# Kernel tuning notes

Measured on AMD Instinct MI355X. Metric: run time of the kernel, lower is better.

## Reference

```python
import jax, jax.numpy as jnp
import numpy as np

G, S = 4, 2
EPS_GN, EPS_COS = 1e-5, 1e-8


def group_norm(x, w, b, groups):
    B, C, H, W = x.shape
    xg = x.reshape(B, groups, C // groups, H, W)
    m = xg.mean(axis=(2, 3, 4), keepdims=True)
    v = ((xg - m) ** 2).mean(axis=(2, 3, 4), keepdims=True)
    xn = ((xg - m) / jnp.sqrt(v + EPS_GN)).reshape(B, C, H, W)
    return xn * w[None, :, None, None] + b[None, :, None, None]


def compute_similarity(x, k=3, dilation=2):
    # cosine similarity (over channels) between each pixel and its 8 dilated
    # neighbors (zero padded, unfold row-major order, center dropped)
    B, C, H, W = x.shape
    pad = (k // 2) * dilation
    xp = jnp.pad(x, ((0, 0), (0, 0), (pad, pad), (pad, pad)))
    cn = jnp.sqrt(jnp.sum(x * x, axis=1))  # (B,H,W)
    sims = []
    for ki in range(k):
        for kj in range(k):
            if ki == k // 2 and kj == k // 2:
                continue
            nb = jax.lax.dynamic_slice(xp, (0, 0, ki * dilation, kj * dilation), (B, C, H, W))
            dot = jnp.sum(x * nb, axis=1)
            nn_ = jnp.sqrt(jnp.sum(nb * nb, axis=1))
            sims.append(dot / jnp.maximum(cn * nn_, EPS_COS))
    return jnp.stack(sims, axis=1)  # (B, k*k-1, H, W)


def conv1x1_bn(x, w, sc, bi):
    # 1x1 conv (no bias) followed by eval-mode BN folded to per-channel scale/shift
    return jnp.einsum('oc,bchw->bohw', w, x) * sc[None, :, None, None] + bi[None, :, None, None]


def pixel_unshuffle(x, r):
    B, C, H, W = x.shape
    return x.reshape(B, C, H // r, r, W // r, r).transpose(0, 1, 3, 5, 2, 4).reshape(B, C * r * r, H // r, W // r)


def pixel_shuffle(x, r):
    B, C, H, W = x.shape
    return x.reshape(B, C // (r * r), r, r, H, W).transpose(0, 1, 4, 2, 5, 3).reshape(B, C // (r * r), H * r, W * r)


def init_pos(dtype):
    h = jnp.arange((-S + 1) / 2, (S - 1) / 2 + 1, dtype=dtype) / S  # [-0.25, 0.25]
    t = jnp.stack(jnp.meshgrid(h, h, indexing='ij')).transpose(0, 2, 1)  # (2,2,2)
    return jnp.tile(t, (1, G, 1)).reshape(1, -1, 1, 1)  # (1, 2*g*s*s, 1, 1)


def grid_sample_border(x, grid):
    # bilinear, align_corners=False, padding_mode='border'
    N, C, H, W = x.shape
    gx = jnp.clip(((grid[..., 0] + 1) * W - 1) / 2, 0.0, W - 1.0)
    gy = jnp.clip(((grid[..., 1] + 1) * H - 1) / 2, 0.0, H - 1.0)
    x0 = jnp.floor(gx)
    y0 = jnp.floor(gy)
    wx = (gx - x0)[..., None]
    wy = (gy - y0)[..., None]
    x0i = x0.astype(jnp.int32)
    y0i = y0.astype(jnp.int32)
    x1i = jnp.minimum(x0i + 1, W - 1)
    y1i = jnp.minimum(y0i + 1, H - 1)
    bi = jnp.arange(N)[:, None, None]
    v00 = x[bi, :, y0i, x0i]  # (N,Ho,Wo,C)
    v01 = x[bi, :, y0i, x1i]
    v10 = x[bi, :, y1i, x0i]
    v11 = x[bi, :, y1i, x1i]
    out = (v00 * (1 - wx) + v01 * wx) * (1 - wy) + (v10 * (1 - wx) + v11 * wx) * wy
    return out.transpose(0, 3, 1, 2)  # (N,C,Ho,Wo)


def sample(x, offset):
    b, _, h, w = offset.shape
    off = offset.reshape(b, 2, -1, h, w)  # (b,2,g*s*s,h,w)
    cw = jnp.arange(w, dtype=x.dtype) + 0.5
    ch = jnp.arange(h, dtype=x.dtype) + 0.5
    coords = jnp.stack(jnp.meshgrid(cw, ch, indexing='ij')).transpose(0, 2, 1)[None, :, None]  # (1,2,1,h,w)
    norm = jnp.array([w, h], dtype=x.dtype).reshape(1, 2, 1, 1, 1)
    coords = 2 * (coords + off) / norm - 1
    grid = pixel_shuffle(coords.reshape(b, -1, h, w), S)  # (b, 2*g, s*h, s*w)
    grid = grid.reshape(b, 2, G, S * h, S * w).transpose(0, 2, 3, 4, 1).reshape(b * G, S * h, S * w, 2)
    C = x.shape[1]
    out = grid_sample_border(x.reshape(b * G, C // G, h, w), grid)
    return out.reshape(b, C, S * h, S * w)


def setup_inputs() -> dict:
    key = jax.random.key(0)
    ks = jax.random.split(key, 24)
    B, C, H, W, CF = 2, 64, 128, 128, 256
    CIN, C2L, C2H = C + 8, 2 * G * S * S, 2 * G
    f = jnp.float32
    return {
        'x_l': jax.random.normal(ks[0], (B, C, H, W), f),
        'x_h': jax.random.normal(ks[1], (B, C, 2 * H, 2 * W), f),
        'feat2sample': jax.random.normal(ks[2], (B, CF, H, W), f),
        'gn_l_w': 1.0 + 0.1 * jax.random.normal(ks[3], (C,), f),
        'gn_l_b': 0.1 * jax.random.normal(ks[4], (C,), f),
        'gn_h_w': 1.0 + 0.1 * jax.random.normal(ks[5], (C,), f),
        'gn_h_b': 0.1 * jax.random.normal(ks[6], (C,), f),
        'w_off': 0.02 * jax.random.normal(ks[7], (C2L, CIN), f),
        's_off': 1.0 + 0.05 * jax.random.normal(ks[8], (C2L,), f),
        'b_off': 0.02 * jax.random.normal(ks[9], (C2L,), f),
        'w_off_h': 0.02 * jax.random.normal(ks[10], (C2H, CIN), f),
        's_off_h': 1.0 + 0.05 * jax.random.normal(ks[11], (C2H,), f),
        'b_off_h': 0.02 * jax.random.normal(ks[12], (C2H,), f),
        'w_ds': 0.02 * jax.random.normal(ks[13], (C2L, CIN), f),
        's_ds': 1.0 + 0.05 * jax.random.normal(ks[14], (C2L,), f),
        'b_ds': 0.02 * jax.random.normal(ks[15], (C2L,), f),
        'w_ds_h': 0.02 * jax.random.normal(ks[16], (C2H, CIN), f),
        's_ds_h': 1.0 + 0.05 * jax.random.normal(ks[17], (C2H,), f),
        'b_ds_h': 0.02 * jax.random.normal(ks[18], (C2H,), f),
    }


def reference(x_l, x_h, feat2sample, gn_l_w, gn_l_b, gn_h_w, gn_h_b,
              w_off, s_off, b_off, w_off_h, s_off_h, b_off_h,
              w_ds, s_ds, b_ds, w_ds_h, s_ds_h, b_ds_h):
    xl = group_norm(x_l, gn_l_w, gn_l_b, x_l.shape[1] // 8)
    xh = group_norm(x_h, gn_h_w, gn_h_b, x_h.shape[1] // 8)
    sim_l = jnp.concatenate([xl, compute_similarity(xl)], axis=1)  # (B, C+8, H, W)
    sim_h = jnp.concatenate([xh, compute_similarity(xh)], axis=1)  # (B, C+8, 2H, 2W)
    off = conv1x1_bn(sim_l, w_off, s_off, b_off) \
        + pixel_unshuffle(conv1x1_bn(sim_h, w_off_h, s_off_h, b_off_h), S)
    gate = jax.nn.sigmoid(conv1x1_bn(sim_l, w_ds, s_ds, b_ds)
                          + pixel_unshuffle(conv1x1_bn(sim_h, w_ds_h, s_ds_h, b_ds_h), S))
    offset = off * gate + init_pos(xl.dtype)  # (B, 2*g*s*s, H, W)
    return sample(feat2sample, offset)
```

## Files before the change

### kernel.cpp

```cpp
#include <hip/hip_runtime.h>
#include <math.h>

#define BATCH 2
#define CCH 64
#define HL 128
#define WL 128
#define HH 256
#define WH 256
#define CFCH 256
#define CIN 72

constexpr long WS_AL   = 0;
constexpr long WS_BL   = 128;
constexpr long WS_AH   = 256;
constexpr long WS_BH   = 384;
constexpr long WS_OFFL = 512;
constexpr long WS_DSL  = WS_OFFL + 1048576;
constexpr long WS_OFFH = WS_DSL + 1048576;
constexpr long WS_DSH  = WS_OFFH + 1048576;
constexpr long WS_CRD  = WS_DSH + 1048576;
constexpr long WS_PART = WS_CRD + 1048576;

__global__ void k_stats1(const float* __restrict__ xl, const float* __restrict__ xh,
                         float* __restrict__ ws) {
  int blk = blockIdx.x;
  const float* x;
  long base;
  int gg, slice;
  if (blk < 256) {
    int g = blk >> 4; slice = blk & 15;
    x = xl; gg = g;
    base = (long)g * 8 * (HL * WL) + (long)slice * 8192;
  } else {
    int id = blk - 256;
    int g = id >> 6; slice = id & 63;
    x = xh; gg = 16 + g;
    base = (long)g * 8 * (HH * WH) + (long)slice * 8192;
  }
  const float4* p = (const float4*)(x + base);
  float s = 0.f, s2 = 0.f;
  #pragma unroll
  for (int k = 0; k < 8; k++) {
    float4 v = p[threadIdx.x + k * 256];
    s  += v.x + v.y + v.z + v.w;
    s2 += v.x * v.x + v.y * v.y + v.z * v.z + v.w * v.w;
  }
  __shared__ float sh1[256], sh2[256];
  sh1[threadIdx.x] = s; sh2[threadIdx.x] = s2;
  __syncthreads();
  for (int off = 128; off > 0; off >>= 1) {
    if (threadIdx.x < off) {
      sh1[threadIdx.x] += sh1[threadIdx.x + off];
      sh2[threadIdx.x] += sh2[threadIdx.x + off];
    }
    __syncthreads();
  }
  if (threadIdx.x == 0) {
    ws[WS_PART + (gg * 64 + slice) * 2]     = sh1[0];
    ws[WS_PART + (gg * 64 + slice) * 2 + 1] = sh2[0];
  }
}

__global__ void k_stats2(const float* __restrict__ gwl, const float* __restrict__ gbl,
                         const float* __restrict__ gwh, const float* __restrict__ gbh,
                         float* __restrict__ ws) {
  int blk = blockIdx.x;
  bool high = blk >= 16;
  int id = blk & 15;
  int b = id >> 3, g = id & 7;
  int gg = high ? 16 + id : id;
  int nsl = high ? 64 : 16;
  long n = high ? (long)8 * HH * WH : (long)8 * HL * WL;
  float s = 0.f, s2 = 0.f;
  for (int i = threadIdx.x; i < nsl; i += 64) {
    s  += ws[WS_PART + (gg * 64 + i) * 2];
    s2 += ws[WS_PART + (gg * 64 + i) * 2 + 1];
  }
  for (int off = 32; off > 0; off >>= 1) {
    s  += __shfl_down(s, off);
    s2 += __shfl_down(s2, off);
  }
  __shared__ float shm[2];
  if (threadIdx.x == 0) { shm[0] = s; shm[1] = s2; }
  __syncthreads();
  if (threadIdx.x < 8) {
    float mean = shm[0] / (float)n;
    float var  = shm[1] / (float)n - mean * mean;
    float inv  = rsqrtf(var + 1e-5f);
    int c = g * 8 + threadIdx.x;
    const float* gw = high ? gwh : gwl;
    const float* gb = high ? gbh : gbl;
    float a  = gw[c] * inv;
    float bb = gb[c] - mean * a;
    float* abase = ws + (high ? WS_AH : WS_AL);
    abase[b * CCH + c] = a;
    abase[128 + b * CCH + c] = bb;
  }
}

template<int HSZ, int WSZ, int NOUT>
__global__ __launch_bounds__(512) void k_head(
                       const float* __restrict__ x,
                       const float* __restrict__ w_off, const float* __restrict__ w_ds,
                       const float* __restrict__ s_off, const float* __restrict__ b_off,
                       const float* __restrict__ s_ds,  const float* __restrict__ b_ds,
                       const float* __restrict__ acoef, const float* __restrict__ bcoef,
                       float* __restrict__ out_off, float* __restrict__ out_ds) {
  constexpr int HW   = HSZ * WSZ;
  constexpr int half = NOUT / 2;
  constexpr int PER  = NOUT / 8;
  __shared__ float wsm[NOUT * CIN];
  __shared__ float xc[CCH * 64];
  __shared__ float psum[8 * 64];
  __shared__ float sims[8 * 64];
  __shared__ float asm_[CCH], bsm_[CCH];

  int tid = threadIdx.x;
  int px = tid & 63;
  int t  = tid >> 6;
  int bid = (blockIdx.x & 7) * (gridDim.x >> 3) + (blockIdx.x >> 3);
  int gpix = bid * 64 + px;
  int xq = gpix % WSZ;
  int yq = (gpix / WSZ) % HSZ;
  int bq = gpix / (WSZ * HSZ);

  for (int i = tid; i < NOUT * CIN; i += 512) {
    int o = i / CIN, c = i % CIN;
    wsm[i] = (o < half) ? w_off[o * CIN + c] : w_ds[(o - half) * CIN + c];
  }
  if (tid < CCH)            asm_[tid] = acoef[bq * CCH + tid];
  else if (tid < 2 * CCH)   bsm_[tid - CCH] = bcoef[bq * CCH + tid - CCH];
  __syncthreads();

  const float* ptr = x + ((long)(bq * CCH)) * HW + yq * WSZ + xq;

  {
    float ss = 0.f;
    #pragma unroll
    for (int k = 0; k < 8; k++) {
      int c = t * 8 + k;
      float v = fmaf(asm_[c], ptr[(long)c * HW], bsm_[c]);
      xc[c * 64 + px] = v;
      ss += v * v;
    }
    psum[t * 64 + px] = ss;
  }
  __syncthreads();

  {
    const int dyv[8] = {-2,-2,-2, 0, 0, 2, 2, 2};
    const int dxv[8] = {-2, 0, 2,-2, 2,-2, 0, 2};
    int dy = dyv[t], dx = dxv[t];
    int yn = yq + dy;
    int xn = xq + dx;
    bool ok = (yn >= 0 && yn < HSZ && xn >= 0 && xn < WSZ);
    float dot = 0.f, nbq = 0.f;
    if (ok) {
      const float* nptr = ptr + (long)dy * WSZ + dx;
      #pragma unroll 16
      for (int c = 0; c < CCH; c++) {
        float nb = fmaf(asm_[c], nptr[(long)c * HW], bsm_[c]);
        float xv = xc[c * 64 + px];
        dot += xv * nb;
        nbq += nb * nb;
      }
    }
    float cs = 0.f;
    #pragma unroll
    for (int tt = 0; tt < 8; tt++) cs += psum[tt * 64 + px];
    float cnc = sqrtf(cs);
    sims[t * 64 + px] = dot / fmaxf(cnc * sqrtf(nbq), 1e-8f);
  }
  __syncthreads();

  {
    float sv[8];
    #pragma unroll
    for (int j = 0; j < 8; j++) sv[j] = sims[j * 64 + px];
    float acc[PER];
    #pragma unroll
    for (int ol = 0; ol < PER; ol++) acc[ol] = 0.f;
    int o0 = t * PER;
    #pragma unroll 4
    for (int c = 0; c < CCH; c += 4) {
      float x0v = xc[(c + 0) * 64 + px];
      float x1v = xc[(c + 1) * 64 + px];
      float x2v = xc[(c + 2) * 64 + px];
      float x3v = xc[(c + 3) * 64 + px];
      #pragma unroll
      for (int ol = 0; ol < PER; ol++) {
        const float4 w4 = *(const float4*)&wsm[(o0 + ol) * CIN + c];
        acc[ol] += w4.x * x0v + w4.y * x1v + w4.z * x2v + w4.w * x3v;
      }
    }
    #pragma unroll
    for (int ol = 0; ol < PER; ol++) {
      const float4 wa = *(const float4*)&wsm[(o0 + ol) * CIN + 64];
      const float4 wb = *(const float4*)&wsm[(o0 + ol) * CIN + 68];
      acc[ol] += wa.x * sv[0] + wa.y * sv[1] + wa.z * sv[2] + wa.w * sv[3]
               + wb.x * sv[4] + wb.y * sv[5] + wb.z * sv[6] + wb.w * sv[7];
    }
    #pragma unroll
    for (int ol = 0; ol < PER; ol++) {
      int o = o0 + ol;
      float v;
      float* dst;
      int oo;
      if (o < half) { v = acc[ol] * s_off[o] + b_off[o];             dst = out_off; oo = o; }
      else          { v = acc[ol] * s_ds[o - half] + b_ds[o - half]; dst = out_ds;  oo = o - half; }
      dst[((long)(bq * half + oo)) * HW + yq * WSZ + xq] = v;
    }
  }
}

__global__ __launch_bounds__(256) void k_combine(float* __restrict__ ws) {
  int idx = blockIdx.x * blockDim.x + threadIdx.x;
  int x = idx & 127;
  int y = (idx >> 7) & 127;
  int sub = (idx >> 14) & 15;
  int b = idx >> 18;
  int sdx = sub & 1, sdy = (sub >> 1) & 1;

  const float* offl = ws + WS_OFFL;
  const float* dsl  = ws + WS_DSL;
  const float* offh = ws + WS_OFFH;
  const float* dsh  = ws + WS_DSH;

  int lidx = idx + b * (16 * HL * WL);
  float ol0 = offl[lidx],               dl0 = dsl[lidx];
  float ol1 = offl[lidx + 16 * HL * WL], dl1 = dsl[lidx + 16 * HL * WL];
  int Y = 2 * y + sdy, X = 2 * x + sdx;
  long h0 = ((long)(b * 8 + (sub >> 2)) * HH + Y) * WH + X;
  long h1 = h0 + (long)4 * HH * WH;
  float oh0 = offh[h0], dh0 = dsh[h0];
  float oh1 = offh[h1], dh1 = dsh[h1];
  float gate0 = 1.f / (1.f + expf(-(dl0 + dh0)));
  float gate1 = 1.f / (1.f + expf(-(dl1 + dh1)));
  float offx = (ol0 + oh0) * gate0 + (sdx ? 0.25f : -0.25f);
  float offy = (ol1 + oh1) * gate1 + (sdy ? 0.25f : -0.25f);
  float gx = fminf(fmaxf((float)x + offx, 0.f), (float)(WL - 1));
  float gy = fminf(fmaxf((float)y + offy, 0.f), (float)(HL - 1));
  float2* crd = (float2*)(ws + WS_CRD);
  crd[idx] = float2{gx, gy};
}

__global__ __launch_bounds__(256, 8) void k_sample(const float* __restrict__ feat,
                                                   const float* __restrict__ ws,
                                                   float* __restrict__ out) {
  __shared__ float sbuf[4 * 512];
  int bid = (blockIdx.x & 7) * 512 + (blockIdx.x >> 3);
  int Y = bid & 255;
  int slab = bid >> 8;
  int chh = slab & 1;
  int g = (slab >> 1) & 3;
  int b = slab >> 3;
  int y = Y >> 1, sdy = Y & 1;
  int w = threadIdx.x >> 6;
  int l = threadIdx.x & 63;

  const float2* crd = (const float2*)(ws + WS_CRD);
  int   pack[4];
  float wxa[4], wya[4];
  bool fb = false;
  #pragma unroll
  for (int j = 0; j < 4; j++) {
    int X = 4 * l + j;
    int x = X >> 1, sdx = X & 1;
    int sub = 4 * g + 2 * sdy + sdx;
    float2 cc = crd[((long)(b * 16 + sub)) * (HL * WL) + y * WL + x];
    float gx = cc.x, gy = cc.y;
    float fx0 = floorf(gx), fy0 = floorf(gy);
    int x0 = (int)fx0, y0 = (int)fy0;
    float wx = gx - fx0, wy = gy - fy0;
    if (x0 >= WL - 1) { x0 = WL - 2; wx = 1.f; }
    if (y0 >= HL - 1) { y0 = HL - 2; wy = 1.f; }
    fb = fb || (y0 < y - 1) || (y0 > y + 1);
    pack[j] = y0 * WL + x0;
    wxa[j] = wx;
    wya[j] = wy;
  }
  int ladj = w * 512 + (1 - y) * 128;

  int row0 = l >> 5;
  int row1 = 2 + row0;
  int fr0 = min(max(y - 1 + row0, 0), HL - 1);
  int fr1 = min(max(y - 1 + row1, 0), HL - 1);
  int x4 = (l & 31) * 4;
  long cbase = (long)(b * CFCH + g * 64 + chh * 32 + w * 8);
  const float* ps0 = feat + (cbase * HL + fr0) * WL + x4;
  const float* ps1 = feat + (cbase * HL + fr1) * WL + x4;
  const float* pg  = feat + cbase * (HL * WL);
  int s0 = w * 512 + row0 * 128 + x4;
  int s1 = w * 512 + row1 * 128 + x4;
  float* po = out + (cbase * HH + Y) * WH + 4 * l;
  const long CSTEP  = (long)HL * WL;
  const long OSTEP  = (long)HH * WH;

  float4 t0 = *(const float4*)ps0;
  float4 t1 = *(const float4*)ps1;
  #pragma unroll 1
  for (int k = 0; k < 8; k++) {
    *(float4*)&sbuf[s0] = t0;
    *(float4*)&sbuf[s1] = t1;
    if (k < 7) {
      ps0 += CSTEP; ps1 += CSTEP;
      t0 = *(const float4*)ps0;
      t1 = *(const float4*)ps1;
    }
    float v[4];
    if (!fb) {
      #pragma unroll
      for (int j = 0; j < 4; j++) {
        int li = pack[j] + ladj;
        float wx = wxa[j], wy = wya[j];
        float s00 = sbuf[li], s01 = sbuf[li + 1];
        float s10 = sbuf[li + 128], s11 = sbuf[li + 129];
        v[j] = (s00 * (1.f - wx) + s01 * wx) * (1.f - wy)
             + (s10 * (1.f - wx) + s11 * wx) * wy;
      }
    } else {
      #pragma unroll
      for (int j = 0; j < 4; j++) {
        const float* pp = pg + pack[j];
        float wx = wxa[j], wy = wya[j];
        float s00 = pp[0], s01 = pp[1];
        float s10 = pp[WL], s11 = pp[WL + 1];
        v[j] = (s00 * (1.f - wx) + s01 * wx) * (1.f - wy)
             + (s10 * (1.f - wx) + s11 * wx) * wy;
      }
    }
    *(float4*)po = make_float4(v[0], v[1], v[2], v[3]);
    po += OSTEP;
    pg += CSTEP;
  }
}

extern "C" void kernel_launch(void* const* d_in, const int* in_sizes, int n_in,
                              void* d_out, int out_size, void* d_ws, size_t ws_size,
                              hipStream_t stream) {
  const float* x_l     = (const float*)d_in[0];
  const float* x_h     = (const float*)d_in[1];
  const float* feat    = (const float*)d_in[2];
  const float* gn_l_w  = (const float*)d_in[3];
  const float* gn_l_b  = (const float*)d_in[4];
  const float* gn_h_w  = (const float*)d_in[5];
  const float* gn_h_b  = (const float*)d_in[6];
  const float* w_off   = (const float*)d_in[7];
  const float* s_off   = (const float*)d_in[8];
  const float* b_off   = (const float*)d_in[9];
  const float* w_off_h = (const float*)d_in[10];
  const float* s_off_h = (const float*)d_in[11];
  const float* b_off_h = (const float*)d_in[12];
  const float* w_ds    = (const float*)d_in[13];
  const float* s_ds    = (const float*)d_in[14];
  const float* b_ds    = (const float*)d_in[15];
  const float* w_ds_h  = (const float*)d_in[16];
  const float* s_ds_h  = (const float*)d_in[17];
  const float* b_ds_h  = (const float*)d_in[18];
  float* ws  = (float*)d_ws;
  float* out = (float*)d_out;

  k_stats1<<<1280, 256, 0, stream>>>(x_l, x_h, ws);
  k_stats2<<<32, 64, 0, stream>>>(gn_l_w, gn_l_b, gn_h_w, gn_h_b, ws);
  k_head<HL, WL, 64><<<(BATCH * HL * WL) / 64, 512, 0, stream>>>(
      x_l, w_off, w_ds, s_off, b_off, s_ds, b_ds,
      ws + WS_AL, ws + WS_BL, ws + WS_OFFL, ws + WS_DSL);
  k_head<HH, WH, 16><<<(BATCH * HH * WH) / 64, 512, 0, stream>>>(
      x_h, w_off_h, w_ds_h, s_off_h, b_off_h, s_ds_h, b_ds_h,
      ws + WS_AH, ws + WS_BH, ws + WS_OFFH, ws + WS_DSH);
  k_combine<<<(BATCH * 16 * HL * WL) / 256, 256, 0, stream>>>(ws);
  k_sample<<<16 * HH, 256, 0, stream>>>(feat, ws, out);
}
```

Measured before the change: 97.82 us.

## Merge both head kernels into one launch; sample two output rows per block

The low- and high-resolution head kernels are combined into one launch that dispatches by block index, with shared memory sized for the larger configuration. This removes a kernel boundary and lets the two heads' blocks overlap. The sampling kernel now produces both sub-rows (sdy=0,1) for each low-res row, so each staged feature tile in shared memory is reused for twice as many outputs and half as many blocks are launched. In exchange, registers per thread rise, and the heads kernel's shared-memory footprint is set by the larger variant for all blocks, which can lower occupancy for the smaller head.

```diff
diff --git a/kernel.cpp b/kernel.cpp
--- a/kernel.cpp
+++ b/kernel.cpp
@@ -98,8 +98,13 @@
   }
 }
 
+__device__ __forceinline__ int head_swz(int blk, int n) {
+  return (blk & 7) * (n >> 3) + (blk >> 3);
+}
+
 template<int HSZ, int WSZ, int NOUT>
-__global__ __launch_bounds__(512) void k_head(
+__device__ __forceinline__ void head_body(
+                       int bid, float* smem,
                        const float* __restrict__ x,
                        const float* __restrict__ w_off, const float* __restrict__ w_ds,
                        const float* __restrict__ s_off, const float* __restrict__ b_off,
@@ -109,16 +114,16 @@
   constexpr int HW   = HSZ * WSZ;
   constexpr int half = NOUT / 2;
   constexpr int PER  = NOUT / 8;
-  __shared__ float wsm[NOUT * CIN];
-  __shared__ float xc[CCH * 64];
-  __shared__ float psum[8 * 64];
-  __shared__ float sims[8 * 64];
-  __shared__ float asm_[CCH], bsm_[CCH];
+  float* wsm  = smem;
+  float* xc   = wsm + NOUT * CIN;
+  float* psum = xc + CCH * 64;
+  float* sims = psum + 512;
+  float* asm_ = sims + 512;
+  float* bsm_ = asm_ + 64;
 
   int tid = threadIdx.x;
   int px = tid & 63;
   int t  = tid >> 6;
-  int bid = (blockIdx.x & 7) * (gridDim.x >> 3) + (blockIdx.x >> 3);
   int gpix = bid * 64 + px;
   int xq = gpix % WSZ;
   int yq = (gpix / WSZ) % HSZ;
@@ -213,6 +218,28 @@
   }
 }
 
+__global__ __launch_bounds__(512) void k_heads(
+    const float* __restrict__ xl, const float* __restrict__ xh,
+    const float* __restrict__ w_off,   const float* __restrict__ w_ds,
+    const float* __restrict__ s_off,   const float* __restrict__ b_off,
+    const float* __restrict__ s_ds,    const float* __restrict__ b_ds,
+    const float* __restrict__ w_off_h, const float* __restrict__ w_ds_h,
+    const float* __restrict__ s_off_h, const float* __restrict__ b_off_h,
+    const float* __restrict__ s_ds_h,  const float* __restrict__ b_ds_h,
+    float* __restrict__ ws) {
+  __shared__ float smem[9856];
+  if (blockIdx.x < 512) {
+    int bid = head_swz(blockIdx.x, 512);
+    head_body<HL, WL, 64>(bid, smem, xl, w_off, w_ds, s_off, b_off, s_ds, b_ds,
+                          ws + WS_AL, ws + WS_BL, ws + WS_OFFL, ws + WS_DSL);
+  } else {
+    int bid = head_swz(blockIdx.x - 512, 2048);
+    head_body<HH, WH, 16>(bid, smem, xh, w_off_h, w_ds_h, s_off_h, b_off_h,
+                          s_ds_h, b_ds_h,
+                          ws + WS_AH, ws + WS_BH, ws + WS_OFFH, ws + WS_DSH);
+  }
+}
+
 __global__ __launch_bounds__(256) void k_combine(float* __restrict__ ws) {
   int idx = blockIdx.x * blockDim.x + threadIdx.x;
   int x = idx & 127;
@@ -244,40 +271,42 @@
   crd[idx] = float2{gx, gy};
 }
 
-__global__ __launch_bounds__(256, 8) void k_sample(const float* __restrict__ feat,
-                                                   const float* __restrict__ ws,
-                                                   float* __restrict__ out) {
+__global__ __launch_bounds__(256) void k_sample(const float* __restrict__ feat,
+                                                const float* __restrict__ ws,
+                                                float* __restrict__ out) {
   __shared__ float sbuf[4 * 512];
-  int bid = (blockIdx.x & 7) * 512 + (blockIdx.x >> 3);
-  int Y = bid & 255;
-  int slab = bid >> 8;
+  int bid = (blockIdx.x & 7) * 256 + (blockIdx.x >> 3);
+  int y = bid & 127;
+  int slab = bid >> 7;
   int chh = slab & 1;
   int g = (slab >> 1) & 3;
   int b = slab >> 3;
-  int y = Y >> 1, sdy = Y & 1;
   int w = threadIdx.x >> 6;
   int l = threadIdx.x & 63;
 
   const float2* crd = (const float2*)(ws + WS_CRD);
-  int   pack[4];
-  float wxa[4], wya[4];
+  int   pack[8];
+  float wxa[8], wya[8];
   bool fb = false;
   #pragma unroll
-  for (int j = 0; j < 4; j++) {
-    int X = 4 * l + j;
-    int x = X >> 1, sdx = X & 1;
-    int sub = 4 * g + 2 * sdy + sdx;
-    float2 cc = crd[((long)(b * 16 + sub)) * (HL * WL) + y * WL + x];
-    float gx = cc.x, gy = cc.y;
-    float fx0 = floorf(gx), fy0 = floorf(gy);
-    int x0 = (int)fx0, y0 = (int)fy0;
-    float wx = gx - fx0, wy = gy - fy0;
-    if (x0 >= WL - 1) { x0 = WL - 2; wx = 1.f; }
-    if (y0 >= HL - 1) { y0 = HL - 2; wy = 1.f; }
-    fb = fb || (y0 < y - 1) || (y0 > y + 1);
-    pack[j] = y0 * WL + x0;
-    wxa[j] = wx;
-    wya[j] = wy;
+  for (int sdy = 0; sdy < 2; sdy++) {
+    #pragma unroll
+    for (int j = 0; j < 4; j++) {
+      int X = 4 * l + j;
+      int x = X >> 1, sdx = X & 1;
+      int sub = 4 * g + 2 * sdy + sdx;
+      float2 cc = crd[((long)(b * 16 + sub)) * (HL * WL) + y * WL + x];
+      float gx = cc.x, gy = cc.y;
+      float fx0 = floorf(gx), fy0 = floorf(gy);
+      int x0 = (int)fx0, y0 = (int)fy0;
+      float wx = gx - fx0, wy = gy - fy0;
+      if (x0 >= WL - 1) { x0 = WL - 2; wx = 1.f; }
+      if (y0 >= HL - 1) { y0 = HL - 2; wy = 1.f; }
+      fb = fb || (y0 < y - 1) || (y0 > y + 1);
+      pack[sdy * 4 + j] = y0 * WL + x0;
+      wxa[sdy * 4 + j] = wx;
+      wya[sdy * 4 + j] = wy;
+    }
   }
   int ladj = w * 512 + (1 - y) * 128;
 
@@ -292,7 +321,8 @@
   const float* pg  = feat + cbase * (HL * WL);
   int s0 = w * 512 + row0 * 128 + x4;
   int s1 = w * 512 + row1 * 128 + x4;
-  float* po = out + (cbase * HH + Y) * WH + 4 * l;
+  float* po0 = out + (cbase * HH + 2 * y) * WH + 4 * l;
+  float* po1 = po0 + WH;
   const long CSTEP  = (long)HL * WL;
   const long OSTEP  = (long)HH * WH;
 
@@ -307,30 +337,31 @@
       t0 = *(const float4*)ps0;
       t1 = *(const float4*)ps1;
     }
-    float v[4];
+    float v[8];
     if (!fb) {
       #pragma unroll
-      for (int j = 0; j < 4; j++) {
-        int li = pack[j] + ladj;
-        float wx = wxa[j], wy = wya[j];
+      for (int q = 0; q < 8; q++) {
+        int li = pack[q] + ladj;
+        float wx = wxa[q], wy = wya[q];
         float s00 = sbuf[li], s01 = sbuf[li + 1];
         float s10 = sbuf[li + 128], s11 = sbuf[li + 129];
-        v[j] = (s00 * (1.f - wx) + s01 * wx) * (1.f - wy)
+        v[q] = (s00 * (1.f - wx) + s01 * wx) * (1.f - wy)
              + (s10 * (1.f - wx) + s11 * wx) * wy;
       }
     } else {
       #pragma unroll
-      for (int j = 0; j < 4; j++) {
-        const float* pp = pg + pack[j];
-        float wx = wxa[j], wy = wya[j];
+      for (int q = 0; q < 8; q++) {
+        const float* pp = pg + pack[q];
+        float wx = wxa[q], wy = wya[q];
         float s00 = pp[0], s01 = pp[1];
         float s10 = pp[WL], s11 = pp[WL + 1];
-        v[j] = (s00 * (1.f - wx) + s01 * wx) * (1.f - wy)
+        v[q] = (s00 * (1.f - wx) + s01 * wx) * (1.f - wy)
              + (s10 * (1.f - wx) + s11 * wx) * wy;
       }
     }
-    *(float4*)po = make_float4(v[0], v[1], v[2], v[3]);
-    po += OSTEP;
+    *(float4*)po0 = make_float4(v[0], v[1], v[2], v[3]);
+    *(float4*)po1 = make_float4(v[4], v[5], v[6], v[7]);
+    po0 += OSTEP; po1 += OSTEP;
     pg += CSTEP;
   }
 }
@@ -362,12 +393,9 @@
 
   k_stats1<<<1280, 256, 0, stream>>>(x_l, x_h, ws);
   k_stats2<<<32, 64, 0, stream>>>(gn_l_w, gn_l_b, gn_h_w, gn_h_b, ws);
-  k_head<HL, WL, 64><<<(BATCH * HL * WL) / 64, 512, 0, stream>>>(
-      x_l, w_off, w_ds, s_off, b_off, s_ds, b_ds,
-      ws + WS_AL, ws + WS_BL, ws + WS_OFFL, ws + WS_DSL);
-  k_head<HH, WH, 16><<<(BATCH * HH * WH) / 64, 512, 0, stream>>>(
-      x_h, w_off_h, w_ds_h, s_off_h, b_off_h, s_ds_h, b_ds_h,
-      ws + WS_AH, ws + WS_BH, ws + WS_OFFH, ws + WS_DSH);
+  k_heads<<<2560, 512, 0, stream>>>(x_l, x_h,
+      w_off, w_ds, s_off, b_off, s_ds, b_ds,
+      w_off_h, w_ds_h, s_off_h, b_off_h, s_ds_h, b_ds_h, ws);
   k_combine<<<(BATCH * 16 * HL * WL) / 256, 256, 0, stream>>>(ws);
-  k_sample<<<16 * HH, 256, 0, stream>>>(feat, ws, out);
-}
+  k_sample<<<2048, 256, 0, stream>>>(feat, ws, out);
+}
```

Measured after the change: 94.39 us. 1.04x faster.
